# Optimization experiments

Hardware: AMD Instinct MI355X
Metric: run time of the kernel (lower is better)

The kernel has to match this reference:

```python
import jax, jax.numpy as jnp
import numpy as np

N = 20000      # nodes
E = 640000     # edges (avg degree 32)
F = 128        # hidden_channels == num_filters
RBF = 64       # num_rbf
H = 8          # num_heads
DH = F // H    # head dim
T = 5          # number of distinct element types present in z
CUT = 5.0      # cutoff_upper (cutoff_lower = 0)


def setup_inputs() -> dict:
    key = jax.random.key(0)
    ks = jax.random.split(key, 20)
    s = 0.05
    inp = {
        "x": jax.random.normal(ks[0], (N, F), jnp.float32),
        "z": jax.random.randint(ks[1], (N,), 0, T, jnp.int32),
        "edge_index": jax.random.randint(ks[2], (2, E), 0, N, jnp.int32),
        "edge_weight": jax.random.uniform(ks[3], (E,), jnp.float32) * CUT,
        "edge_attr": jax.random.normal(ks[4], (E, RBF), jnp.float32),
        # ElemConv params
        "lin1_w": jax.random.normal(ks[5], (F, F), jnp.float32) / np.sqrt(F),
        "f_w1": jax.random.normal(ks[6], (F, RBF), jnp.float32) / np.sqrt(RBF),
        "f_b1": jnp.zeros((F,), jnp.float32),
        "f_w2": jax.random.normal(ks[7], (F, F), jnp.float32) / np.sqrt(F),
        "f_b2": jnp.zeros((F,), jnp.float32),
        # ElemAttn params
        "q_w": jax.random.normal(ks[8], (F, F), jnp.float32) / np.sqrt(F),
        "q_b": jax.random.normal(ks[9], (F,), jnp.float32) * s,
        "k_w": jax.random.normal(ks[10], (F, F), jnp.float32) / np.sqrt(F),
        "k_b": jax.random.normal(ks[11], (F,), jnp.float32) * s,
        "v_w": jax.random.normal(ks[12], (F, F), jnp.float32) / np.sqrt(F),
        "v_b": jax.random.normal(ks[13], (F,), jnp.float32) * s,
        "o1_w": jax.random.normal(ks[14], (F, F), jnp.float32) / np.sqrt(F),
        "o1_b": jax.random.normal(ks[15], (F,), jnp.float32) * s,
        "o2_w": jax.random.normal(ks[16], (F, F), jnp.float32) / np.sqrt(F),
        "o2_b": jax.random.normal(ks[17], (F,), jnp.float32) * s,
    }
    return inp


def reference(x, z, edge_index, edge_weight, edge_attr,
              lin1_w, f_w1, f_b1, f_w2, f_b2,
              q_w, q_b, k_w, k_b, v_w, v_b, o1_w, o1_b, o2_w, o2_b):
    silu = jax.nn.silu
    src, dst = edge_index[0], edge_index[1]

    # ---- ElemConv ----
    # CosineCutoff (cutoff_lower = 0)
    C = 0.5 * (jnp.cos(edge_weight * (jnp.pi / CUT)) + 1.0)
    C = C * (edge_weight < CUT).astype(x.dtype)
    # filter_net(edge_attr) * C
    W = silu(edge_attr @ f_w1.T + f_b1) @ f_w2.T + f_b2          # [E, F]
    W = W * C[:, None]
    xl = x @ lin1_w.T                                             # [N, F]
    msg = xl[src] * W                                             # [E, F]
    # aggregate by unique (z_j, dst) pair == dense [N, T] slot grid
    seg = dst * T + z[src]                                        # [E]
    y = jax.ops.segment_sum(msg, seg, num_segments=N * T).reshape(N, T, F)
    cnt = jax.ops.segment_sum(jnp.ones((E,), x.dtype), seg, num_segments=N * T)
    pm = (cnt > 0).astype(x.dtype).reshape(N, T)                  # presence mask

    # ---- ElemAttn (block-diagonal per target node over present slots) ----
    q = (y @ q_w.T + q_b).reshape(N, T, H, DH)
    k = (y @ k_w.T + k_b).reshape(N, T, H, DH)
    v = (y @ v_w.T + v_b).reshape(N, T, H, DH)
    attn = silu(jnp.einsum('nihd,njhd->nhij', q, k))              # [N, H, T, T]
    attn = attn * (pm[:, None, :, None] * pm[:, None, None, :])
    out = jnp.einsum('nhij,njhd->nihd', attn, v).reshape(N, T, F)
    out = out @ o1_w.T + o1_b                                     # [N, T, F]
    node = jnp.einsum('ntf,nt->nf', out, pm)                      # scatter-add by node
    return silu(node @ o2_w.T + o2_b)                             # [N, F]
```

## Files before the change

kernel.cpp:

```cpp
#include <hip/hip_runtime.h>

#define N_NODES 20000
#define E_EDGES 640000
#define F_DIM 128
#define RBF_DIM 64
#define T_TYPES 5
#define NSEG (N_NODES * T_TYPES)
#define EPB 128

typedef __attribute__((ext_vector_type(8))) short short8;
typedef __attribute__((ext_vector_type(4))) float f32x4;

__device__ __forceinline__ float silu_f(float x) { return x / (1.0f + __expf(-x)); }

__device__ __forceinline__ ushort f2bf(float f) {
  unsigned u = __float_as_uint(f);
  u += 0x7fffu + ((u >> 16) & 1u);
  return (ushort)(u >> 16);
}
__device__ __forceinline__ float bf2f(ushort u) {
  return __uint_as_float(((unsigned)u) << 16);
}
__device__ __forceinline__ unsigned cvt_pk(float lo, float hi) {
  unsigned r;
  asm("v_cvt_pk_bf16_f32 %0, %1, %2" : "=v"(r) : "v"(lo), "v"(hi));
  return r;
}
union S8U4 {
  short8 s;
  unsigned u[4];
};

__global__ __launch_bounds__(256) void prep_kernel(
    const float* __restrict__ w1, const float* __restrict__ w2,
    const float* __restrict__ qw, const float* __restrict__ kw,
    const float* __restrict__ vw, ushort* __restrict__ w1b,
    ushort* __restrict__ w2b, ushort* __restrict__ qwb,
    ushort* __restrict__ kwb, ushort* __restrict__ vwb) {
  int i = blockIdx.x * 256 + threadIdx.x;
  if (i < F_DIM * RBF_DIM) w1b[i] = f2bf(w1[i]);
  if (i < F_DIM * F_DIM) {
    w2b[i] = f2bf(w2[i]);
    qwb[i] = f2bf(qw[i]);
    kwb[i] = f2bf(kw[i]);
    vwb[i] = f2bf(vw[i]);
  }
}

__global__ __launch_bounds__(256) void hist_rank_kernel(
    const int* __restrict__ srcp, const int* __restrict__ dstp,
    const int* __restrict__ z, int* __restrict__ hist, int* __restrict__ rnk) {
  int e = blockIdx.x * 256 + threadIdx.x;
  int s = srcp[e];
  int seg = dstp[e] * T_TYPES + z[s];
  rnk[e] = atomicAdd(&hist[seg], 1);
}

__global__ __launch_bounds__(256) void scan1_kernel(const int* __restrict__ hist,
                                                    int* __restrict__ offs,
                                                    int* __restrict__ bsums) {
  __shared__ int lds[256];
  int tid = threadIdx.x;
  int base = blockIdx.x * 1024 + tid * 4;
  int v[4];
  int s = 0;
#pragma unroll
  for (int i = 0; i < 4; ++i) {
    v[i] = (base + i < NSEG) ? hist[base + i] : 0;
    s += v[i];
  }
  lds[tid] = s;
  __syncthreads();
  for (int d = 1; d < 256; d <<= 1) {
    int t = (tid >= d) ? lds[tid - d] : 0;
    __syncthreads();
    lds[tid] += t;
    __syncthreads();
  }
  int excl = lds[tid] - s;
#pragma unroll
  for (int i = 0; i < 4; ++i) {
    if (base + i < NSEG) offs[base + i] = excl;
    excl += v[i];
  }
  if (tid == 255) bsums[blockIdx.x] = lds[255];
}

__global__ __launch_bounds__(128) void scan2_kernel(int* __restrict__ bsums,
                                                    int nb) {
  __shared__ int lds[128];
  int tid = threadIdx.x;
  int v = (tid < nb) ? bsums[tid] : 0;
  lds[tid] = v;
  __syncthreads();
  for (int d = 1; d < 128; d <<= 1) {
    int t = (tid >= d) ? lds[tid - d] : 0;
    __syncthreads();
    lds[tid] += t;
    __syncthreads();
  }
  if (tid < nb) bsums[tid] = lds[tid] - v;
}

__global__ __launch_bounds__(256) void scan3_kernel(int* __restrict__ offs,
                                                    const int* __restrict__ bsums) {
  int tid = threadIdx.x;
  int base = blockIdx.x * 1024 + tid * 4;
  int add = bsums[blockIdx.x];
#pragma unroll
  for (int i = 0; i < 4; ++i)
    if (base + i < NSEG) offs[base + i] += add;
}

__global__ __launch_bounds__(256) void scatter_kernel(
    const int* __restrict__ srcp, const int* __restrict__ dstp,
    const int* __restrict__ z, const int* __restrict__ offs,
    const int* __restrict__ rnk, int* __restrict__ perm) {
  int e = blockIdx.x * 256 + threadIdx.x;
  int s = srcp[e];
  int seg = dstp[e] * T_TYPES + z[s];
  perm[offs[seg] + rnk[e]] = e;
}

__global__ __launch_bounds__(128) void lin1_kernel(const float* __restrict__ x,
                                                   const float* __restrict__ w,
                                                   ushort* __restrict__ xlb) {
  __shared__ float xs[8 * 128];
  int tid = threadIdx.x;
  int n0 = blockIdx.x * 8;
  const float4* xg = (const float4*)(x + (size_t)n0 * 128);
  float4* xs4 = (float4*)xs;
  for (int i = tid; i < 256; i += 128) xs4[i] = xg[i];
  __syncthreads();
  int f = tid;
  float acc[8] = {};
  const float4* w4 = (const float4*)(w + (size_t)f * 128);
  for (int j4 = 0; j4 < 32; ++j4) {
    float4 wv = w4[j4];
#pragma unroll
    for (int n = 0; n < 8; ++n) {
      float4 xv = xs4[n * 32 + j4];
      acc[n] += wv.x * xv.x + wv.y * xv.y + wv.z * xv.z + wv.w * xv.w;
    }
  }
  for (int n = 0; n < 8; ++n) xlb[(size_t)(n0 + n) * 128 + f] = f2bf(acc[n]);
}

__global__ __launch_bounds__(256, 4) void edge_mfma_kernel(
    const float* __restrict__ edge_attr, const int* __restrict__ srcp,
    const int* __restrict__ dstp, const float* __restrict__ ewp,
    const int* __restrict__ z, const int* __restrict__ perm,
    const ushort* __restrict__ w1b, const float* __restrict__ b1,
    const ushort* __restrict__ w2b, const float* __restrict__ b2,
    const ushort* __restrict__ xlb, float* __restrict__ y) {
  __shared__ ushort hs[128 * 136];
  __shared__ float sC[EPB];
  __shared__ int srcoff[EPB];
  __shared__ int sseg[EPB];
  __shared__ unsigned long long smask[2];

  const int tid = threadIdx.x;
  const int e0 = blockIdx.x * EPB;
  const int lane = tid & 63;
  const int w = tid >> 6;
  const int wm = w >> 1, wn = w & 1;
  const int lr = lane & 15, lh = lane >> 4;

  int prow[4];
#pragma unroll
  for (int fm = 0; fm < 4; ++fm) prow[fm] = perm[e0 + wm * 64 + fm * 16 + lr];

  float rb1[4], rb2[4];
#pragma unroll
  for (int fc = 0; fc < 4; ++fc) {
    int n = wn * 64 + fc * 16 + lr;
    rb1[fc] = b1[n];
    rb2[fc] = b2[n];
  }

  if (tid < EPB) {
    int e = perm[e0 + tid];
    int s = srcp[e];
    srcoff[tid] = s * 128;
    sseg[tid] = dstp[e] * T_TYPES + z[s];
    float wd = ewp[e];
    float c = 0.5f * (__cosf(wd * 0.6283185307179586f) + 1.0f);
    sC[tid] = (wd < 5.0f) ? c : 0.0f;
  }

  f32x4 acc[4][4] = {};
#pragma unroll
  for (int ks = 0; ks < 2; ++ks) {
    const int k0 = ks * 32;
    short8 af[4], bfr[4];
#pragma unroll
    for (int fm = 0; fm < 4; ++fm) {
      const float* ap = edge_attr + (size_t)prow[fm] * 64 + k0 + lh * 8;
      float4 a0 = *(const float4*)ap;
      float4 a1 = *(const float4*)(ap + 4);
      S8U4 t;
      t.u[0] = cvt_pk(a0.x, a0.y);
      t.u[1] = cvt_pk(a0.z, a0.w);
      t.u[2] = cvt_pk(a1.x, a1.y);
      t.u[3] = cvt_pk(a1.z, a1.w);
      af[fm] = t.s;
    }
#pragma unroll
    for (int fc = 0; fc < 4; ++fc)
      bfr[fc] = *(const short8*)(w1b + (size_t)(wn * 64 + fc * 16 + lr) * 64 +
                                 k0 + lh * 8);
#pragma unroll
    for (int fm = 0; fm < 4; ++fm)
#pragma unroll
      for (int fc = 0; fc < 4; ++fc)
        acc[fm][fc] = __builtin_amdgcn_mfma_f32_16x16x32_bf16(
            af[fm], bfr[fc], acc[fm][fc], 0, 0, 0);
  }

#pragma unroll
  for (int fm = 0; fm < 4; ++fm) {
#pragma unroll
    for (int fc = 0; fc < 4; ++fc) {
#pragma unroll
      for (int rp = 0; rp < 4; rp += 2) {
        int ml0 = wm * 64 + fm * 16 + lh * 4 + rp;
        int ml1 = ml0 + 1;
        int n = wn * 64 + fc * 16 + lr;
        float h0 = silu_f(acc[fm][fc][rp] + rb1[fc]);
        float h1 = silu_f(acc[fm][fc][rp + 1] + rb1[fc]);
        unsigned u = cvt_pk(h0, h1);
        hs[(ml0 * 256 + ((n * 2) ^ ((ml0 & 7) << 4))) >> 1] = (ushort)u;
        hs[(ml1 * 256 + ((n * 2) ^ ((ml1 & 7) << 4))) >> 1] = (ushort)(u >> 16);
      }
    }
  }
  __syncthreads();

  if (tid < EPB) {
    int head = (tid == 0) || (sseg[tid] != sseg[tid - 1]);
    unsigned long long m = __ballot(head);
    if ((tid & 63) == 0) smask[tid >> 6] = m;
  }

  f32x4 acc2[4][4] = {};
#pragma unroll
  for (int ks = 0; ks < 4; ++ks) {
    const int k0 = ks * 32;
    short8 af[4], bfr[4];
#pragma unroll
    for (int fm = 0; fm < 4; ++fm) {
      int ml = wm * 64 + fm * 16 + lr;
      int byte_in_row = (k0 * 2 + lh * 16) ^ ((ml & 7) << 4);
      af[fm] = *(const short8*)&hs[(ml * 256 + byte_in_row) >> 1];
    }
#pragma unroll
    for (int fc = 0; fc < 4; ++fc)
      bfr[fc] = *(const short8*)(w2b + (size_t)(wn * 64 + fc * 16 + lr) * 128 +
                                 k0 + lh * 8);
#pragma unroll
    for (int fm = 0; fm < 4; ++fm)
#pragma unroll
      for (int fc = 0; fc < 4; ++fc)
        acc2[fm][fc] = __builtin_amdgcn_mfma_f32_16x16x32_bf16(
            af[fm], bfr[fc], acc2[fm][fc], 0, 0, 0);
  }
  __syncthreads();

#pragma unroll
  for (int fm = 0; fm < 4; ++fm) {
#pragma unroll
    for (int rp = 0; rp < 4; rp += 2) {
      int ml0 = wm * 64 + fm * 16 + lh * 4 + rp;
      float c0 = sC[ml0], c1 = sC[ml0 + 1];
#pragma unroll
      for (int fc = 0; fc < 4; ++fc) {
        int n = wn * 64 + fc * 16 + lr;
        float v0 = (acc2[fm][fc][rp] + rb2[fc]) * c0;
        float v1 = (acc2[fm][fc][rp + 1] + rb2[fc]) * c1;
        *(unsigned*)&hs[n * 136 + ml0] = cvt_pk(v0, v1);
      }
    }
  }
  __syncthreads();

  {
    int cp = tid & 63;
    int q = tid >> 6;
    int rbase = q * 32;
    int c0 = cp * 2;
    unsigned mm = (unsigned)(smask[q >> 1] >> ((q & 1) * 32));
    float a0 = 0.0f, a1 = 0.0f;
    int cur = sseg[rbase];
    bool first = true;
#pragma unroll
    for (int it = 0; it < 4; ++it) {
      int r0 = rbase + it * 8;
      short8 m0 = *(const short8*)&hs[c0 * 136 + r0];
      short8 m1 = *(const short8*)&hs[(c0 + 1) * 136 + r0];
      unsigned xv[8];
#pragma unroll
      for (int j = 0; j < 8; ++j)
        xv[j] = *(const unsigned*)&xlb[(size_t)srcoff[r0 + j] + c0];
#pragma unroll
      for (int j = 0; j < 8; ++j) {
        int rr = it * 8 + j;
        if (rr && ((mm >> rr) & 1u)) {
          float* yp = &y[(size_t)cur * 128 + c0];
          if (first) {
            atomicAdd(yp, a0);
            atomicAdd(yp + 1, a1);
            first = false;
          } else {
            yp[0] = a0;
            yp[1] = a1;
          }
          a0 = a1 = 0.0f;
          cur = sseg[r0 + j];
        }
        a0 += bf2f((ushort)m0[j]) * bf2f((ushort)xv[j]);
        a1 += bf2f((ushort)m1[j]) * bf2f((ushort)(xv[j] >> 16));
      }
    }
    float* yp = &y[(size_t)cur * 128 + c0];
    atomicAdd(yp, a0);
    atomicAdd(yp + 1, a1);
  }
}

#define QS 136
#define NB 16
__global__ __launch_bounds__(256) void attn_out_kernel(
    const float* __restrict__ y, const int* __restrict__ hist,
    const ushort* __restrict__ qwb, const ushort* __restrict__ kwb,
    const ushort* __restrict__ vwb, const float* __restrict__ qb,
    const float* __restrict__ kb, const float* __restrict__ vb,
    const float* __restrict__ o1w, const float* __restrict__ o1b,
    const float* __restrict__ o2w, const float* __restrict__ o2b,
    float* __restrict__ outp) {
  __shared__ ushort bufA[80 * QS];
  __shared__ ushort bufB[80 * QS];
  __shared__ float aap[NB * 8 * 2 * 5];
  __shared__ float pmv[80];
  __shared__ float snpm[NB];
  __shared__ float sxb[3][128];

  const int tid = threadIdx.x;
  const int n0 = blockIdx.x * NB;
  const int row0 = n0 * T_TYPES;
  const int lane = tid & 63;
  const int w = tid >> 6;
  const int lr = lane & 15, lh = lane >> 4;

  if (tid < 128) {
    sxb[0][tid] = qb[tid];
    sxb[1][tid] = kb[tid];
    sxb[2][tid] = vb[tid];
  }
  if (tid < 80) pmv[tid] = (hist[(size_t)row0 + tid] > 0) ? 1.0f : 0.0f;

  short8 A[4][5];
#pragma unroll
  for (int ksi = 0; ksi < 4; ++ksi) {
#pragma unroll
    for (int fm = 0; fm < 5; ++fm) {
      const float* ap =
          y + (size_t)(row0 + fm * 16 + lr) * 128 + ksi * 32 + lh * 8;
      float4 a0 = *(const float4*)ap;
      float4 a1 = *(const float4*)(ap + 4);
      S8U4 t;
      t.u[0] = cvt_pk(a0.x, a0.y);
      t.u[1] = cvt_pk(a0.z, a0.w);
      t.u[2] = cvt_pk(a1.x, a1.y);
      t.u[3] = cvt_pk(a1.z, a1.w);
      A[ksi][fm] = t.s;
    }
  }
  __syncthreads();
  if (tid < NB) {
    float s = 0.0f;
#pragma unroll
    for (int t = 0; t < 5; ++t) s += pmv[tid * 5 + t];
    snpm[tid] = s;
  }

  auto do_proj = [&](const ushort* __restrict__ Wb, const float* bias_row,
                     ushort* __restrict__ dst) {
    f32x4 acc[5][2] = {};
#pragma unroll
    for (int ksi = 0; ksi < 4; ++ksi) {
      short8 B[2];
#pragma unroll
      for (int fc = 0; fc < 2; ++fc)
        B[fc] = *(const short8*)(Wb + (size_t)(w * 32 + fc * 16 + lr) * 128 +
                                 ksi * 32 + lh * 8);
#pragma unroll
      for (int fm = 0; fm < 5; ++fm)
#pragma unroll
        for (int fc = 0; fc < 2; ++fc)
          acc[fm][fc] = __builtin_amdgcn_mfma_f32_16x16x32_bf16(
              A[ksi][fm], B[fc], acc[fm][fc], 0, 0, 0);
    }
#pragma unroll
    for (int fm = 0; fm < 5; ++fm)
#pragma unroll
      for (int fc = 0; fc < 2; ++fc)
#pragma unroll
        for (int rp = 0; rp < 4; rp += 2) {
          int rrow = fm * 16 + lh * 4 + rp;
          int col = w * 32 + fc * 16 + lr;
          float v0 = acc[fm][fc][rp] + bias_row[col];
          float v1 = acc[fm][fc][rp + 1] + bias_row[col];
          unsigned u = cvt_pk(v0, v1);
          dst[rrow * QS + col] = (ushort)u;
          dst[(rrow + 1) * QS + col] = (ushort)(u >> 16);
        }
  };

  do_proj(qwb, sxb[0], bufA);
  do_proj(kwb, sxb[1], bufB);
  __syncthreads();

  {
    int n = tid >> 4, h = (tid >> 1) & 7, g = tid & 1;
    int i0 = g ? 3 : 0;
    int cnt = g ? 2 : 3;
    float kv[5][16];
#pragma unroll
    for (int j = 0; j < 5; ++j) {
      short8 v0 = *(const short8*)&bufB[(n * 5 + j) * QS + h * 16];
      short8 v1 = *(const short8*)&bufB[(n * 5 + j) * QS + h * 16 + 8];
#pragma unroll
      for (int d = 0; d < 8; ++d) {
        kv[j][d] = bf2f((ushort)v0[d]);
        kv[j][d + 8] = bf2f((ushort)v1[d]);
      }
    }
    float a[5] = {};
    for (int ii = 0; ii < cnt; ++ii) {
      int i = i0 + ii;
      float qv[16];
      short8 q0 = *(const short8*)&bufA[(n * 5 + i) * QS + h * 16];
      short8 q1 = *(const short8*)&bufA[(n * 5 + i) * QS + h * 16 + 8];
#pragma unroll
      for (int d = 0; d < 8; ++d) {
        qv[d] = bf2f((ushort)q0[d]);
        qv[d + 8] = bf2f((ushort)q1[d]);
      }
      float pmi = pmv[n * 5 + i];
#pragma unroll
      for (int j = 0; j < 5; ++j) {
        float dd = 0.0f;
#pragma unroll
        for (int d = 0; d < 16; ++d) dd += qv[d] * kv[j][d];
        a[j] += pmi * silu_f(dd);
      }
    }
#pragma unroll
    for (int j = 0; j < 5; ++j) aap[((n * 8 + h) * 2 + g) * 5 + j] = a[j];
  }
  __syncthreads();

  do_proj(vwb, sxb[2], bufA);
  __syncthreads();

  float* sf = (float*)bufB;
  {
    int n = tid >> 4;
    int o = tid & 15;
    int f0 = o * 8;
    int h = f0 >> 4;
    float acc8[8] = {};
#pragma unroll
    for (int j = 0; j < 5; ++j) {
      float a = (aap[((n * 8 + h) * 2 + 0) * 5 + j] +
                 aap[((n * 8 + h) * 2 + 1) * 5 + j]) *
                pmv[n * 5 + j];
      short8 vv8 = *(const short8*)&bufA[(n * 5 + j) * QS + f0];
#pragma unroll
      for (int d = 0; d < 8; ++d) acc8[d] += a * bf2f((ushort)vv8[d]);
    }
    float* op = sf + n * 128 + f0;
    *(float4*)op = make_float4(acc8[0], acc8[1], acc8[2], acc8[3]);
    *(float4*)(op + 4) = make_float4(acc8[4], acc8[5], acc8[6], acc8[7]);
  }
  __syncthreads();

  float* t1f = (float*)bufA;
  {
    int f = tid & 127, half = tid >> 7;
    const float4* wg = (const float4*)(o1w + (size_t)f * 128);
    const float4* s4 = (const float4*)sf;
    float acc[8] = {};
    for (int j4 = 0; j4 < 32; ++j4) {
      float4 wv = wg[j4];
#pragma unroll
      for (int nn = 0; nn < 8; ++nn) {
        float4 sv = s4[(half * 8 + nn) * 32 + j4];
        acc[nn] += wv.x * sv.x + wv.y * sv.y + wv.z * sv.z + wv.w * sv.w;
      }
    }
    float bb = o1b[f];
#pragma unroll
    for (int nn = 0; nn < 8; ++nn) {
      int n = half * 8 + nn;
      t1f[n * 128 + f] = acc[nn] + snpm[n] * bb;
    }
  }
  __syncthreads();

  {
    int f = tid & 127, half = tid >> 7;
    const float4* wg = (const float4*)(o2w + (size_t)f * 128);
    const float4* t4 = (const float4*)t1f;
    float acc[8] = {};
    for (int j4 = 0; j4 < 32; ++j4) {
      float4 wv = wg[j4];
#pragma unroll
      for (int nn = 0; nn < 8; ++nn) {
        float4 tv = t4[(half * 8 + nn) * 32 + j4];
        acc[nn] += wv.x * tv.x + wv.y * tv.y + wv.z * tv.z + wv.w * tv.w;
      }
    }
    float bb = o2b[f];
#pragma unroll
    for (int nn = 0; nn < 8; ++nn) {
      int n = half * 8 + nn;
      outp[(size_t)(n0 + n) * 128 + f] = silu_f(acc[nn] + bb);
    }
  }
}

extern "C" void kernel_launch(void* const* d_in, const int* in_sizes, int n_in,
                              void* d_out, int out_size, void* d_ws, size_t ws_size,
                              hipStream_t stream) {
  const float* x = (const float*)d_in[0];
  const int* z = (const int*)d_in[1];
  const int* ei = (const int*)d_in[2];
  const float* ew = (const float*)d_in[3];
  const float* ea = (const float*)d_in[4];
  const float* lin1_w = (const float*)d_in[5];
  const float* fw1 = (const float*)d_in[6];
  const float* fb1 = (const float*)d_in[7];
  const float* fw2 = (const float*)d_in[8];
  const float* fb2 = (const float*)d_in[9];
  const float* qw = (const float*)d_in[10];
  const float* qb = (const float*)d_in[11];
  const float* kw = (const float*)d_in[12];
  const float* kb = (const float*)d_in[13];
  const float* vw = (const float*)d_in[14];
  const float* vb = (const float*)d_in[15];
  const float* o1w = (const float*)d_in[16];
  const float* o1b = (const float*)d_in[17];
  const float* o2w = (const float*)d_in[18];
  const float* o2b = (const float*)d_in[19];
  float* outp = (float*)d_out;
  float* ws = (float*)d_ws;

  float* y = ws;
  ushort* xlb = (ushort*)(y + (size_t)NSEG * F_DIM);
  ushort* w1b = xlb + (size_t)N_NODES * F_DIM;
  ushort* w2b = w1b + F_DIM * RBF_DIM;
  ushort* qwb = w2b + F_DIM * F_DIM;
  ushort* kwb = qwb + F_DIM * F_DIM;
  ushort* vwb = kwb + F_DIM * F_DIM;
  int* hist = (int*)(vwb + F_DIM * F_DIM);
  int* offs = hist + NSEG;
  int* bsums = offs + NSEG;
  int* rnk = bsums + 128;
  int* perm = rnk + E_EDGES;

  const int* srcp = ei;
  const int* dstp = ei + E_EDGES;
  const int NB_SCAN = (NSEG + 1023) / 1024;

  hipMemsetAsync(y, 0, (size_t)NSEG * F_DIM * sizeof(float), stream);
  hipMemsetAsync(hist, 0, (size_t)NSEG * sizeof(int), stream);

  prep_kernel<<<64, 256, 0, stream>>>(fw1, fw2, qw, kw, vw, w1b, w2b, qwb, kwb, vwb);
  hist_rank_kernel<<<E_EDGES / 256, 256, 0, stream>>>(srcp, dstp, z, hist, rnk);
  scan1_kernel<<<NB_SCAN, 256, 0, stream>>>(hist, offs, bsums);
  scan2_kernel<<<1, 128, 0, stream>>>(bsums, NB_SCAN);
  scan3_kernel<<<NB_SCAN, 256, 0, stream>>>(offs, bsums);
  scatter_kernel<<<E_EDGES / 256, 256, 0, stream>>>(srcp, dstp, z, offs, rnk, perm);
  lin1_kernel<<<N_NODES / 8, 128, 0, stream>>>(x, lin1_w, xlb);
  edge_mfma_kernel<<<E_EDGES / EPB, 256, 0, stream>>>(ea, srcp, dstp, ew, z, perm,
                                                      w1b, fb1, w2b, fb2, xlb, y);
  attn_out_kernel<<<N_NODES / NB, 256, 0, stream>>>(y, hist, qwb, kwb, vwb, qb, kb,
                                                    vb, o1w, o1b, o2w, o2b, outp);
}
```

Baseline: 339.1 us.

## Use bf16 MFMA for output projections and remap blocks across XCDs

Replaces the scalar fp32 o1/o2 projection loops in the attention-output kernel with bf16 MFMA 16x16x32 instructions. The o1/o2 weights are pre-converted to bf16, and the intermediates are kept in bf16 in LDS. Block indices in both the edge kernel and the attention kernel are remapped so that contiguous chunks of work land on the same XCD, which is meant to improve L2 locality. The projections lose some precision by moving from fp32 to bf16.

Result: faster. 323.7 us (-4.6%).

```diff
diff --git a/kernel.cpp b/kernel.cpp
--- a/kernel.cpp
+++ b/kernel.cpp
@@ -34,9 +34,11 @@
 __global__ __launch_bounds__(256) void prep_kernel(
     const float* __restrict__ w1, const float* __restrict__ w2,
     const float* __restrict__ qw, const float* __restrict__ kw,
-    const float* __restrict__ vw, ushort* __restrict__ w1b,
+    const float* __restrict__ vw, const float* __restrict__ o1w,
+    const float* __restrict__ o2w, ushort* __restrict__ w1b,
     ushort* __restrict__ w2b, ushort* __restrict__ qwb,
-    ushort* __restrict__ kwb, ushort* __restrict__ vwb) {
+    ushort* __restrict__ kwb, ushort* __restrict__ vwb,
+    ushort* __restrict__ o1wb, ushort* __restrict__ o2wb) {
   int i = blockIdx.x * 256 + threadIdx.x;
   if (i < F_DIM * RBF_DIM) w1b[i] = f2bf(w1[i]);
   if (i < F_DIM * F_DIM) {
@@ -44,6 +46,8 @@
     qwb[i] = f2bf(qw[i]);
     kwb[i] = f2bf(kw[i]);
     vwb[i] = f2bf(vw[i]);
+    o1wb[i] = f2bf(o1w[i]);
+    o2wb[i] = f2bf(o2w[i]);
   }
 }
 
@@ -160,7 +164,8 @@
   __shared__ unsigned long long smask[2];
 
   const int tid = threadIdx.x;
-  const int e0 = blockIdx.x * EPB;
+  const int bid = (blockIdx.x & 7) * 625 + (blockIdx.x >> 3);
+  const int e0 = bid * EPB;
   const int lane = tid & 63;
   const int w = tid >> 6;
   const int wm = w >> 1, wn = w & 1;
@@ -334,8 +339,8 @@
     const ushort* __restrict__ qwb, const ushort* __restrict__ kwb,
     const ushort* __restrict__ vwb, const float* __restrict__ qb,
     const float* __restrict__ kb, const float* __restrict__ vb,
-    const float* __restrict__ o1w, const float* __restrict__ o1b,
-    const float* __restrict__ o2w, const float* __restrict__ o2b,
+    const ushort* __restrict__ o1wb, const float* __restrict__ o1b,
+    const ushort* __restrict__ o2wb, const float* __restrict__ o2b,
     float* __restrict__ outp) {
   __shared__ ushort bufA[80 * QS];
   __shared__ ushort bufB[80 * QS];
@@ -345,7 +350,10 @@
   __shared__ float sxb[3][128];
 
   const int tid = threadIdx.x;
-  const int n0 = blockIdx.x * NB;
+  const int xcd = blockIdx.x & 7;
+  const int loc = blockIdx.x >> 3;
+  const int bid = (xcd < 2 ? xcd * 157 : 314 + (xcd - 2) * 156) + loc;
+  const int n0 = bid * NB;
   const int row0 = n0 * T_TYPES;
   const int lane = tid & 63;
   const int w = tid >> 6;
@@ -463,7 +471,6 @@
   do_proj(vwb, sxb[2], bufA);
   __syncthreads();
 
-  float* sf = (float*)bufB;
   {
     int n = tid >> 4;
     int o = tid & 15;
@@ -479,53 +486,61 @@
 #pragma unroll
       for (int d = 0; d < 8; ++d) acc8[d] += a * bf2f((ushort)vv8[d]);
     }
-    float* op = sf + n * 128 + f0;
-    *(float4*)op = make_float4(acc8[0], acc8[1], acc8[2], acc8[3]);
-    *(float4*)(op + 4) = make_float4(acc8[4], acc8[5], acc8[6], acc8[7]);
-  }
-  __syncthreads();
-
-  float* t1f = (float*)bufA;
+    S8U4 t;
+    t.u[0] = cvt_pk(acc8[0], acc8[1]);
+    t.u[1] = cvt_pk(acc8[2], acc8[3]);
+    t.u[2] = cvt_pk(acc8[4], acc8[5]);
+    t.u[3] = cvt_pk(acc8[6], acc8[7]);
+    *(short8*)&bufB[n * QS + f0] = t.s;
+  }
+  __syncthreads();
+
   {
-    int f = tid & 127, half = tid >> 7;
-    const float4* wg = (const float4*)(o1w + (size_t)f * 128);
-    const float4* s4 = (const float4*)sf;
-    float acc[8] = {};
-    for (int j4 = 0; j4 < 32; ++j4) {
-      float4 wv = wg[j4];
-#pragma unroll
-      for (int nn = 0; nn < 8; ++nn) {
-        float4 sv = s4[(half * 8 + nn) * 32 + j4];
-        acc[nn] += wv.x * sv.x + wv.y * sv.y + wv.z * sv.z + wv.w * sv.w;
-      }
-    }
-    float bb = o1b[f];
-#pragma unroll
-    for (int nn = 0; nn < 8; ++nn) {
-      int n = half * 8 + nn;
-      t1f[n * 128 + f] = acc[nn] + snpm[n] * bb;
+    f32x4 acc[2] = {};
+#pragma unroll
+    for (int ksi = 0; ksi < 4; ++ksi) {
+      short8 af = *(const short8*)&bufB[lr * QS + ksi * 32 + lh * 8];
+      short8 B0 = *(const short8*)(o1wb + (size_t)(w * 32 + lr) * 128 +
+                                   ksi * 32 + lh * 8);
+      short8 B1 = *(const short8*)(o1wb + (size_t)(w * 32 + 16 + lr) * 128 +
+                                   ksi * 32 + lh * 8);
+      acc[0] = __builtin_amdgcn_mfma_f32_16x16x32_bf16(af, B0, acc[0], 0, 0, 0);
+      acc[1] = __builtin_amdgcn_mfma_f32_16x16x32_bf16(af, B1, acc[1], 0, 0, 0);
+    }
+#pragma unroll
+    for (int fc = 0; fc < 2; ++fc) {
+      int col = w * 32 + fc * 16 + lr;
+      float bb = o1b[col];
+#pragma unroll
+      for (int r = 0; r < 4; ++r) {
+        int row = lh * 4 + r;
+        bufA[row * QS + col] = f2bf(acc[fc][r] + snpm[row] * bb);
+      }
     }
   }
   __syncthreads();
 
   {
-    int f = tid & 127, half = tid >> 7;
-    const float4* wg = (const float4*)(o2w + (size_t)f * 128);
-    const float4* t4 = (const float4*)t1f;
-    float acc[8] = {};
-    for (int j4 = 0; j4 < 32; ++j4) {
-      float4 wv = wg[j4];
-#pragma unroll
-      for (int nn = 0; nn < 8; ++nn) {
-        float4 tv = t4[(half * 8 + nn) * 32 + j4];
-        acc[nn] += wv.x * tv.x + wv.y * tv.y + wv.z * tv.z + wv.w * tv.w;
-      }
-    }
-    float bb = o2b[f];
-#pragma unroll
-    for (int nn = 0; nn < 8; ++nn) {
-      int n = half * 8 + nn;
-      outp[(size_t)(n0 + n) * 128 + f] = silu_f(acc[nn] + bb);
+    f32x4 acc[2] = {};
+#pragma unroll
+    for (int ksi = 0; ksi < 4; ++ksi) {
+      short8 af = *(const short8*)&bufA[lr * QS + ksi * 32 + lh * 8];
+      short8 B0 = *(const short8*)(o2wb + (size_t)(w * 32 + lr) * 128 +
+                                   ksi * 32 + lh * 8);
+      short8 B1 = *(const short8*)(o2wb + (size_t)(w * 32 + 16 + lr) * 128 +
+                                   ksi * 32 + lh * 8);
+      acc[0] = __builtin_amdgcn_mfma_f32_16x16x32_bf16(af, B0, acc[0], 0, 0, 0);
+      acc[1] = __builtin_amdgcn_mfma_f32_16x16x32_bf16(af, B1, acc[1], 0, 0, 0);
+    }
+#pragma unroll
+    for (int fc = 0; fc < 2; ++fc) {
+      int col = w * 32 + fc * 16 + lr;
+      float bb = o2b[col];
+#pragma unroll
+      for (int r = 0; r < 4; ++r) {
+        int row = lh * 4 + r;
+        outp[(size_t)(n0 + row) * 128 + col] = silu_f(acc[fc][r] + bb);
+      }
     }
   }
 }
@@ -563,7 +578,9 @@
   ushort* qwb = w2b + F_DIM * F_DIM;
   ushort* kwb = qwb + F_DIM * F_DIM;
   ushort* vwb = kwb + F_DIM * F_DIM;
-  int* hist = (int*)(vwb + F_DIM * F_DIM);
+  ushort* o1wb = vwb + F_DIM * F_DIM;
+  ushort* o2wb = o1wb + F_DIM * F_DIM;
+  int* hist = (int*)(o2wb + F_DIM * F_DIM);
   int* offs = hist + NSEG;
   int* bsums = offs + NSEG;
   int* rnk = bsums + 128;
@@ -576,7 +593,8 @@
   hipMemsetAsync(y, 0, (size_t)NSEG * F_DIM * sizeof(float), stream);
   hipMemsetAsync(hist, 0, (size_t)NSEG * sizeof(int), stream);
 
-  prep_kernel<<<64, 256, 0, stream>>>(fw1, fw2, qw, kw, vw, w1b, w2b, qwb, kwb, vwb);
+  prep_kernel<<<64, 256, 0, stream>>>(fw1, fw2, qw, kw, vw, o1w, o2w, w1b, w2b,
+                                      qwb, kwb, vwb, o1wb, o2wb);
   hist_rank_kernel<<<E_EDGES / 256, 256, 0, stream>>>(srcp, dstp, z, hist, rnk);
   scan1_kernel<<<NB_SCAN, 256, 0, stream>>>(hist, offs, bsums);
   scan2_kernel<<<1, 128, 0, stream>>>(bsums, NB_SCAN);
@@ -586,5 +604,5 @@
   edge_mfma_kernel<<<E_EDGES / EPB, 256, 0, stream>>>(ea, srcp, dstp, ew, z, perm,
                                                       w1b, fb1, w2b, fb2, xlb, y);
   attn_out_kernel<<<N_NODES / NB, 256, 0, stream>>>(y, hist, qwb, kwb, vwb, qb, kb,
-                                                    vb, o1w, o1b, o2w, o2b, outp);
-}
+                                                    vb, o1wb, o1b, o2wb, o2b, outp);
+}
```
